# Optimization experiments

Hardware: AMD Instinct MI355X
Metric: run time of the kernel (lower is better)

## Reference

```python
import jax, jax.numpy as jnp
import numpy as np

EMBED_DIM = 1024
NUM_HEADS = 16
HEAD_DIM = EMBED_DIM // NUM_HEADS


def setup_inputs() -> dict:
    key = jax.random.key(0)
    ks = jax.random.split(key, 5)
    s = 1.0 / np.sqrt(EMBED_DIM)
    x = jax.random.normal(ks[0], (2, 2048, EMBED_DIM), dtype=jnp.float32)
    Wq = jax.random.normal(ks[1], (EMBED_DIM, EMBED_DIM), dtype=jnp.float32) * s
    Wk = jax.random.normal(ks[2], (EMBED_DIM, EMBED_DIM), dtype=jnp.float32) * s
    Wv = jax.random.normal(ks[3], (EMBED_DIM, EMBED_DIM), dtype=jnp.float32) * s
    Wo = jax.random.normal(ks[4], (EMBED_DIM, EMBED_DIM), dtype=jnp.float32) * s
    z = jnp.zeros((EMBED_DIM,), dtype=jnp.float32)
    return {"x": x, "Wq": Wq, "bq": z, "Wk": Wk, "bk": z, "Wv": Wv, "bv": z, "Wo": Wo, "bo": z}


def reference(x, Wq, bq, Wk, bk, Wv, bv, Wo, bo):
    B, S, E = x.shape
    H, D = NUM_HEADS, HEAD_DIM
    # projections; weights stored as [in, out] so y = x @ W + b
    q = (x @ Wq + bq).reshape(B, S, H, D).transpose(0, 2, 1, 3)  # [B,H,S,D]
    k = (x @ Wk + bk).reshape(B, S, H, D).transpose(0, 2, 1, 3)
    v = (x @ Wv + bv).reshape(B, S, H, D).transpose(0, 2, 1, 3)
    scores = jnp.einsum('bhqd,bhkd->bhqk', q, k) / jnp.sqrt(jnp.float32(D))
    attn = jax.nn.softmax(scores, axis=-1)
    out = jnp.einsum('bhqk,bhkd->bhqd', attn, v)  # [B,H,S,D]
    out = out.transpose(0, 2, 1, 3).reshape(B, S, E)
    return out @ Wo + bo
```

## Files before the change

### kernel.cpp

```cpp
#include <hip/hip_runtime.h>
#include <cstdint>
#include <cstddef>

typedef __attribute__((ext_vector_type(8))) short bf16x8;
typedef __attribute__((ext_vector_type(4))) float f32x4;
typedef __attribute__((ext_vector_type(16))) float f32x16;
typedef __attribute__((ext_vector_type(4))) unsigned int u32x4;
typedef __attribute__((ext_vector_type(2))) unsigned int u32x2;

__device__ __forceinline__ unsigned short f2bf(float f) {
    union { float f; unsigned int u; } c; c.f = f;
    unsigned int r = c.u + 0x7FFFu + ((c.u >> 16) & 1u);
    return (unsigned short)(r >> 16);
}
__device__ __forceinline__ unsigned int pack2bf(float a, float b) {
    return (unsigned int)f2bf(a) | ((unsigned int)f2bf(b) << 16);
}
__device__ __forceinline__ unsigned int cvtpk(float lo, float hi) {
    unsigned int r;
    asm("v_cvt_pk_bf16_f32 %0, %1, %2" : "=v"(r) : "v"(lo), "v"(hi));
    return r;
}
__device__ __forceinline__ void gload16(const void* g, void* l) {
    __builtin_amdgcn_global_load_lds((const __attribute__((address_space(1))) void*)g,
                                     (__attribute__((address_space(3))) void*)l, 16, 0, 0);
}
__device__ __forceinline__ float tmax16(const f32x16& v) {
    float a0 = fmaxf(v[0], v[1]),   a1 = fmaxf(v[2], v[3]);
    float a2 = fmaxf(v[4], v[5]),   a3 = fmaxf(v[6], v[7]);
    float a4 = fmaxf(v[8], v[9]),   a5 = fmaxf(v[10], v[11]);
    float a6 = fmaxf(v[12], v[13]), a7 = fmaxf(v[14], v[15]);
    float b0 = fmaxf(a0, a1), b1 = fmaxf(a2, a3);
    float b2 = fmaxf(a4, a5), b3 = fmaxf(a6, a7);
    return fmaxf(fmaxf(b0, b1), fmaxf(b2, b3));
}
__device__ __forceinline__ float tsum16(const float* p) {
    float a0 = p[0] + p[1],   a1 = p[2] + p[3];
    float a2 = p[4] + p[5],   a3 = p[6] + p[7];
    float a4 = p[8] + p[9],   a5 = p[10] + p[11];
    float a6 = p[12] + p[13], a7 = p[14] + p[15];
    float b0 = a0 + a1, b1 = a2 + a3, b2 = a4 + a5, b3 = a6 + a7;
    return (b0 + b1) + (b2 + b3);
}

__global__ __launch_bounds__(256) void cvt_kernel(const float* __restrict__ x,
    const float* __restrict__ w0, const float* __restrict__ w1,
    const float* __restrict__ w2, const float* __restrict__ w3,
    unsigned short* __restrict__ xdst, unsigned short* __restrict__ wdst) {
    __shared__ unsigned short sm[64][68];
    const int bid = blockIdx.x;
    const int tid = threadIdx.x;
    if (bid >= 1024) {
        int e = ((bid - 1024) * 256 + tid) * 8;
        const float4* s4 = reinterpret_cast<const float4*>(x + e);
        float4 a = s4[0], b = s4[1];
        u32x4 o;
        o.x = pack2bf(a.x, a.y); o.y = pack2bf(a.z, a.w);
        o.z = pack2bf(b.x, b.y); o.w = pack2bf(b.z, b.w);
        *reinterpret_cast<u32x4*>(xdst + e) = o;
        return;
    }
    int z = bid >> 8, xb = bid & 255;
    const float* src = (z == 0) ? w0 : (z == 1) ? w1 : (z == 2) ? w2 : w3;
    unsigned short* dst = wdst + (size_t)z * 1048576;
    int n0 = (xb & 15) * 64;
    int k0 = (xb >> 4) * 64;
    #pragma unroll
    for (int i = 0; i < 4; i++) {
        int e = i * 1024 + tid * 4;
        int r = e >> 6, c = e & 63;
        float4 v = *reinterpret_cast<const float4*>(src + (size_t)(k0 + r) * 1024 + n0 + c);
        u32x2 p; p.x = pack2bf(v.x, v.y); p.y = pack2bf(v.z, v.w);
        *reinterpret_cast<u32x2*>(&sm[r][c]) = p;
    }
    __syncthreads();
    #pragma unroll
    for (int i = 0; i < 4; i++) {
        int e = i * 1024 + tid * 4;
        int n = e >> 6, kk = e & 63;
        u32x2 p;
        p.x = (unsigned)sm[kk][n]     | ((unsigned)sm[kk + 1][n] << 16);
        p.y = (unsigned)sm[kk + 2][n] | ((unsigned)sm[kk + 3][n] << 16);
        *reinterpret_cast<u32x2*>(dst + (size_t)(n0 + n) * 1024 + k0 + kk) = p;
    }
}

__device__ __forceinline__ void gemm128_main(
    const unsigned short* __restrict__ A, const unsigned short* __restrict__ Wt,
    int m0, int n0, int tid,
    unsigned short* Asm, unsigned short* Bsm,
    f32x4 acc[4][4])
{
    const int lane = tid & 63;
    const int w = tid >> 6;
    const int wm = w >> 1, wn = w & 1;
    const int lr = lane & 15, lg = lane >> 4;
    for (int k0 = 0; k0 < 1024; k0 += 64) {
        __syncthreads();
        #pragma unroll
        for (int i = 0; i < 4; i++) {
            int L = (i * 4 + w) * 64 + lane;
            int r = L >> 3, cs = L & 7;
            int c = cs ^ (r & 7);
            gload16(A  + (size_t)(m0 + r) * 1024 + k0 + c * 8, Asm + (i * 4 + w) * 512);
            gload16(Wt + (size_t)(n0 + r) * 1024 + k0 + c * 8, Bsm + (i * 4 + w) * 512);
        }
        __syncthreads();
        #pragma unroll
        for (int ks = 0; ks < 2; ks++) {
            bf16x8 af[4], bfr[4];
            #pragma unroll
            for (int t = 0; t < 4; t++) {
                int Ra = wm * 64 + t * 16 + lr;
                af[t]  = *reinterpret_cast<const bf16x8*>(Asm + Ra * 64 + ((ks * 4 + lg) ^ (Ra & 7)) * 8);
                int Rb = wn * 64 + t * 16 + lr;
                bfr[t] = *reinterpret_cast<const bf16x8*>(Bsm + Rb * 64 + ((ks * 4 + lg) ^ (Rb & 7)) * 8);
            }
            #pragma unroll
            for (int mt = 0; mt < 4; mt++) {
                #pragma unroll
                for (int nt = 0; nt < 4; nt++)
                    acc[mt][nt] = __builtin_amdgcn_mfma_f32_16x16x32_bf16(af[mt], bfr[nt], acc[mt][nt], 0, 0, 0);
            }
        }
    }
}

__global__ __launch_bounds__(256) void gemm_qkv_kernel(
    const unsigned short* __restrict__ A, const unsigned short* __restrict__ WtBase,
    const float* __restrict__ bq, const float* __restrict__ bk, const float* __restrict__ bv,
    unsigned short* __restrict__ Qo, unsigned short* __restrict__ Ko, unsigned short* __restrict__ Vto)
{
    __shared__ unsigned short Asm[8192];
    __shared__ unsigned short Bsm[8192];
    const int bid = blockIdx.x;
    const int wg = (bid & 7) * 96 + (bid >> 3);
    const int z = wg >> 8;
    const int rem = wg & 255;
    const int m0 = (rem >> 3) * 128, n0 = (rem & 7) * 128;
    const unsigned short* Wt = WtBase + (size_t)z * 1048576;
    const float* bias = (z == 0) ? bq : (z == 1) ? bk : bv;
    const int tid = threadIdx.x, lane = tid & 63, w = tid >> 6;
    const int wm = w >> 1, wn = w & 1, lr = lane & 15, lg = lane >> 4;
    f32x4 acc[4][4];
    f32x4 zero4 = {0.f, 0.f, 0.f, 0.f};
    #pragma unroll
    for (int i = 0; i < 4; i++)
        #pragma unroll
        for (int j = 0; j < 4; j++) acc[i][j] = zero4;
    gemm128_main(A, Wt, m0, n0, tid, Asm, Bsm, acc);

    const float qs = 0.125f * 1.44269504088896341f;
    #pragma unroll
    for (int mt = 0; mt < 4; mt++) {
        #pragma unroll
        for (int nt = 0; nt < 4; nt++) {
            int gn = n0 + wn * 64 + nt * 16 + lr;
            int h = gn >> 6, d = gn & 63;
            int rb = m0 + wm * 64 + mt * 16 + lg * 4;
            int b_ = rb >> 11, s = rb & 2047;
            float bv_ = bias[gn];
            if (z == 2) {
                u32x2 p;
                p.x = pack2bf(acc[mt][nt][0] + bv_, acc[mt][nt][1] + bv_);
                p.y = pack2bf(acc[mt][nt][2] + bv_, acc[mt][nt][3] + bv_);
                *reinterpret_cast<u32x2*>(Vto + ((size_t)(b_ * 16 + h) * 64 + d) * 2048 + s) = p;
            } else {
                unsigned short* dst = (z == 0) ? Qo : Ko;
                float sc_ = (z == 0) ? qs : 1.0f;
                #pragma unroll
                for (int r = 0; r < 4; r++)
                    dst[((size_t)(b_ * 16 + h) * 2048 + (s + r)) * 64 + d] = f2bf((acc[mt][nt][r] + bv_) * sc_);
            }
        }
    }
}

__global__ __launch_bounds__(256, 2) void attn_kernel(
    const unsigned short* __restrict__ Qg,
    const unsigned short* __restrict__ Kg,
    const unsigned short* __restrict__ Vtg,
    unsigned short* __restrict__ Og)
{
    __shared__ unsigned short Ksm[128][72];
    __shared__ unsigned short Vsm[64][136];

    const int tid = threadIdx.x, lane = tid & 63, w = tid >> 6;
    const int l31 = lane & 31, L = lane >> 5;
    const int bh = blockIdx.y, q0 = blockIdx.x * 128;
    const size_t kvbase = (size_t)bh * (2048 * 64);
    const size_t vtbase = (size_t)bh * (64 * 2048);

    {
        u32x4 qr[4];
        #pragma unroll
        for (int i = 0; i < 4; i++) {
            int ck = i * 256 + tid; int r = ck >> 3, c = (ck & 7) * 8;
            qr[i] = *reinterpret_cast<const u32x4*>(Qg + kvbase + (size_t)(q0 + r) * 64 + c);
        }
        #pragma unroll
        for (int i = 0; i < 4; i++) {
            int ck = i * 256 + tid; int r = ck >> 3, c = (ck & 7) * 8;
            *reinterpret_cast<u32x4*>(&Ksm[r][c]) = qr[i];
        }
    }
    __syncthreads();
    bf16x8 qf[4];
    #pragma unroll
    for (int ds = 0; ds < 4; ds++)
        qf[ds] = *reinterpret_cast<const bf16x8*>(&Ksm[w * 32 + l31][ds * 16 + L * 8]);
    __syncthreads();

    f32x16 oacc[2];
    #pragma unroll
    for (int dt = 0; dt < 2; dt++)
        #pragma unroll
        for (int j = 0; j < 16; j++) oacc[dt][j] = 0.f;
    float m_run = -3.0e38f, l_run = 0.f;

    f32x16 z16;
    #pragma unroll
    for (int j = 0; j < 16; j++) z16[j] = 0.f;

    u32x4 kreg[4], vreg[4];
#define LOAD_TILE(KV0)                                                                      \
    _Pragma("unroll")                                                                       \
    for (int i = 0; i < 4; i++) {                                                           \
        int ck = i * 256 + tid; int r = ck >> 3, c = (ck & 7) * 8;                          \
        kreg[i] = *reinterpret_cast<const u32x4*>(Kg + kvbase + (size_t)((KV0) + r) * 64 + c); \
        int dv = ck >> 4, cv = (ck & 15) * 8;                                               \
        vreg[i] = *reinterpret_cast<const u32x4*>(Vtg + vtbase + (size_t)dv * 2048 + (KV0) + cv); \
    }

    LOAD_TILE(0)
    for (int kt = 0; kt < 16; kt++) {
        #pragma unroll
        for (int i = 0; i < 4; i++) {
            int ck = i * 256 + tid; int r = ck >> 3, c = (ck & 7) * 8;
            int rp = r ^ (((((r >> 2) ^ (r >> 3)) & 1)) * 12);
            *reinterpret_cast<u32x4*>(&Ksm[rp][c]) = kreg[i];
            int dv = ck >> 4, cv = (ck & 15) * 8;
            *reinterpret_cast<u32x4*>(&Vsm[dv][cv]) = vreg[i];
        }
        __syncthreads();
        int kvn = (kt < 15) ? (kt + 1) * 128 : 0;
        LOAD_TILE(kvn)

        f32x16 sc[4];
        #pragma unroll
        for (int nt = 0; nt < 4; nt++) {
            {
                bf16x8 kf = *reinterpret_cast<const bf16x8*>(&Ksm[nt * 32 + l31][L * 8]);
                sc[nt] = __builtin_amdgcn_mfma_f32_32x32x16_bf16(kf, qf[0], z16, 0, 0, 0);
            }
            #pragma unroll
            for (int ds = 1; ds < 4; ds++) {
                bf16x8 kf = *reinterpret_cast<const bf16x8*>(&Ksm[nt * 32 + l31][ds * 16 + L * 8]);
                sc[nt] = __builtin_amdgcn_mfma_f32_32x32x16_bf16(kf, qf[ds], sc[nt], 0, 0, 0);
            }
        }

        float pmax = fmaxf(fmaxf(tmax16(sc[0]), tmax16(sc[1])),
                           fmaxf(tmax16(sc[2]), tmax16(sc[3])));
        pmax = fmaxf(pmax, __shfl_xor(pmax, 32));

        if (__any(pmax - m_run > 8.0f)) {
            float mnew = fmaxf(m_run, pmax);
            float f = __builtin_amdgcn_exp2f(m_run - mnew);
            l_run *= f;
            #pragma unroll
            for (int dt = 0; dt < 2; dt++)
                #pragma unroll
                for (int j = 0; j < 16; j++) oacc[dt][j] *= f;
            m_run = mnew;
        }

        float psum = 0.f;
        unsigned pdw[4][4][2];
        #pragma unroll
        for (int nt = 0; nt < 4; nt++) {
            float p[16];
            #pragma unroll
            for (int j = 0; j < 16; j++)
                p[j] = __builtin_amdgcn_exp2f(sc[nt][j] - m_run);
            psum += tsum16(p);
            #pragma unroll
            for (int a = 0; a < 4; a++) {
                pdw[nt][a][0] = cvtpk(p[4 * a + 0], p[4 * a + 1]);
                pdw[nt][a][1] = cvtpk(p[4 * a + 2], p[4 * a + 3]);
            }
        }
        psum += __shfl_xor(psum, 32);
        l_run += psum;

        #pragma unroll
        for (int kt2 = 0; kt2 < 8; kt2++) {
            const int nt = kt2 >> 1, c2 = (kt2 & 1) * 2;
            u32x4 pf4;
            pf4.x = pdw[nt][c2][0];
            pf4.y = pdw[nt][c2][1];
            pf4.z = pdw[nt][c2 + 1][0];
            pf4.w = pdw[nt][c2 + 1][1];
            bf16x8 pfr = *reinterpret_cast<bf16x8*>(&pf4);
            #pragma unroll
            for (int dt = 0; dt < 2; dt++) {
                bf16x8 vf = *reinterpret_cast<const bf16x8*>(&Vsm[dt * 32 + l31][kt2 * 16 + L * 8]);
                oacc[dt] = __builtin_amdgcn_mfma_f32_32x32x16_bf16(vf, pfr, oacc[dt], 0, 0, 0);
            }
        }
        __syncthreads();
    }
#undef LOAD_TILE

    float inv = 1.0f / l_run;
    const int b_ = bh >> 4, h = bh & 15;
    const int s = q0 + w * 32 + l31;
    unsigned short* orow = Og + ((size_t)b_ * 2048 + s) * 1024 + h * 64;
    #pragma unroll
    for (int dt = 0; dt < 2; dt++) {
        #pragma unroll
        for (int g = 0; g < 4; g++) {
            u32x2 pp;
            pp.x = cvtpk(oacc[dt][4 * g + 0] * inv, oacc[dt][4 * g + 1] * inv);
            pp.y = cvtpk(oacc[dt][4 * g + 2] * inv, oacc[dt][4 * g + 3] * inv);
            *reinterpret_cast<u32x2*>(orow + dt * 32 + g * 8 + 4 * L) = pp;
        }
    }
}

__global__ __launch_bounds__(256) void gemm_out_kernel(
    const unsigned short* __restrict__ A, const unsigned short* __restrict__ Wt,
    const float* __restrict__ bias, float* __restrict__ out)
{
    __shared__ unsigned short Asm[8192];
    __shared__ unsigned short Bsm[8192];
    const int bid = blockIdx.x;
    const int wg = (bid & 7) * 32 + (bid >> 3);
    const int m0 = (wg >> 3) * 128, n0 = (wg & 7) * 128;
    const int tid = threadIdx.x, lane = tid & 63, w = tid >> 6;
    const int wm = w >> 1, wn = w & 1, lr = lane & 15, lg = lane >> 4;
    f32x4 acc[4][4];
    f32x4 zero4 = {0.f, 0.f, 0.f, 0.f};
    #pragma unroll
    for (int i = 0; i < 4; i++)
        #pragma unroll
        for (int j = 0; j < 4; j++) acc[i][j] = zero4;
    gemm128_main(A, Wt, m0, n0, tid, Asm, Bsm, acc);
    #pragma unroll
    for (int mt = 0; mt < 4; mt++) {
        #pragma unroll
        for (int nt = 0; nt < 4; nt++) {
            int gn = n0 + wn * 64 + nt * 16 + lr;
            float bv_ = bias[gn];
            int rb = m0 + wm * 64 + mt * 16 + lg * 4;
            #pragma unroll
            for (int r = 0; r < 4; r++)
                out[(size_t)(rb + r) * 1024 + gn] = acc[mt][nt][r] + bv_;
        }
    }
}

extern "C" void kernel_launch(void* const* d_in, const int* in_sizes, int n_in,
                              void* d_out, int out_size, void* d_ws, size_t ws_size,
                              hipStream_t stream) {
    const float* x  = (const float*)d_in[0];
    const float* Wq = (const float*)d_in[1];
    const float* bq = (const float*)d_in[2];
    const float* Wk = (const float*)d_in[3];
    const float* bk = (const float*)d_in[4];
    const float* Wv = (const float*)d_in[5];
    const float* bv = (const float*)d_in[6];
    const float* Wo = (const float*)d_in[7];
    const float* bo = (const float*)d_in[8];
    float* out = (float*)d_out;

    if (ws_size < (size_t)25165824 * 2) return;
    unsigned short* ws  = (unsigned short*)d_ws;
    unsigned short* xbf = ws;
    unsigned short* wt  = ws + 4194304;
    unsigned short* Qb  = ws + 8388608;
    unsigned short* Kb  = ws + 12582912;
    unsigned short* Vtb = ws + 16777216;
    unsigned short* Ob  = ws + 20971520;

    cvt_kernel<<<3072, 256, 0, stream>>>(x, Wq, Wk, Wv, Wo, xbf, wt);
    gemm_qkv_kernel<<<768, 256, 0, stream>>>(xbf, wt, bq, bk, bv, Qb, Kb, Vtb);
    attn_kernel<<<dim3(16, 32), 256, 0, stream>>>(Qb, Kb, Vtb, Ob);
    gemm_out_kernel<<<256, 256, 0, stream>>>(Ob, wt + 3 * 1048576, bo, out);
}
```

Before: 129.1 us.

## Double-buffer GEMM K-loop with 32-wide stages and raise occupancy hint

Restructures the shared GEMM main loop into a two-buffer ping-pong pipeline over K-slices of 32. The next slice is loaded asynchronously into LDS while the current one runs through MFMA, which should hide global-load latency behind compute. The LDS swizzle is changed to match the narrower 32-column rows. Launch bounds now request three blocks per SM for the QKV and output GEMMs, which may force register limits or spills. Barriers per K step rise, and each MFMA round has less work between syncs.

```diff
diff --git a/kernel.cpp b/kernel.cpp
--- a/kernel.cpp
+++ b/kernel.cpp
@@ -85,6 +85,40 @@
     }
 }
 
+__device__ __forceinline__ void gemm128_stage(
+    const unsigned short* __restrict__ A, const unsigned short* __restrict__ Wt,
+    int m0, int n0, int tid, int k0,
+    unsigned short* Ad, unsigned short* Bd)
+{
+    #pragma unroll
+    for (int i = 0; i < 2; i++) {
+        int L = i * 256 + tid;
+        int r = L >> 2, cs = L & 3;
+        int c = cs ^ ((r & 3) ^ ((r >> 2) & 3));
+        gload16(A  + (size_t)(m0 + r) * 1024 + k0 + c * 8, Ad + L * 8);
+        gload16(Wt + (size_t)(n0 + r) * 1024 + k0 + c * 8, Bd + L * 8);
+    }
+}
+__device__ __forceinline__ void gemm128_compute(
+    const unsigned short* Ac, const unsigned short* Bc,
+    int wm, int wn, int lr, int lg,
+    f32x4 acc[4][4])
+{
+    bf16x8 af[4], bfr[4];
+    #pragma unroll
+    for (int t = 0; t < 4; t++) {
+        int Ra = wm * 64 + t * 16 + lr;
+        af[t]  = *reinterpret_cast<const bf16x8*>(Ac + Ra * 32 + (lg ^ ((Ra & 3) ^ ((Ra >> 2) & 3))) * 8);
+        int Rb = wn * 64 + t * 16 + lr;
+        bfr[t] = *reinterpret_cast<const bf16x8*>(Bc + Rb * 32 + (lg ^ ((Rb & 3) ^ ((Rb >> 2) & 3))) * 8);
+    }
+    #pragma unroll
+    for (int mt = 0; mt < 4; mt++) {
+        #pragma unroll
+        for (int nt = 0; nt < 4; nt++)
+            acc[mt][nt] = __builtin_amdgcn_mfma_f32_16x16x32_bf16(af[mt], bfr[nt], acc[mt][nt], 0, 0, 0);
+    }
+}
 __device__ __forceinline__ void gemm128_main(
     const unsigned short* __restrict__ A, const unsigned short* __restrict__ Wt,
     int m0, int n0, int tid,
@@ -95,38 +129,23 @@
     const int w = tid >> 6;
     const int wm = w >> 1, wn = w & 1;
     const int lr = lane & 15, lg = lane >> 4;
-    for (int k0 = 0; k0 < 1024; k0 += 64) {
+    unsigned short* A0 = Asm;        unsigned short* B0 = Bsm;
+    unsigned short* A1 = Asm + 4096; unsigned short* B1 = Bsm + 4096;
+
+    gemm128_stage(A, Wt, m0, n0, tid, 0, A0, B0);
+    __syncthreads();
+    for (int t = 0; t < 32; t += 2) {
+        gemm128_stage(A, Wt, m0, n0, tid, (t + 1) * 32, A1, B1);
+        gemm128_compute(A0, B0, wm, wn, lr, lg, acc);
         __syncthreads();
-        #pragma unroll
-        for (int i = 0; i < 4; i++) {
-            int L = (i * 4 + w) * 64 + lane;
-            int r = L >> 3, cs = L & 7;
-            int c = cs ^ (r & 7);
-            gload16(A  + (size_t)(m0 + r) * 1024 + k0 + c * 8, Asm + (i * 4 + w) * 512);
-            gload16(Wt + (size_t)(n0 + r) * 1024 + k0 + c * 8, Bsm + (i * 4 + w) * 512);
-        }
+        if (t + 2 < 32)
+            gemm128_stage(A, Wt, m0, n0, tid, (t + 2) * 32, A0, B0);
+        gemm128_compute(A1, B1, wm, wn, lr, lg, acc);
         __syncthreads();
-        #pragma unroll
-        for (int ks = 0; ks < 2; ks++) {
-            bf16x8 af[4], bfr[4];
-            #pragma unroll
-            for (int t = 0; t < 4; t++) {
-                int Ra = wm * 64 + t * 16 + lr;
-                af[t]  = *reinterpret_cast<const bf16x8*>(Asm + Ra * 64 + ((ks * 4 + lg) ^ (Ra & 7)) * 8);
-                int Rb = wn * 64 + t * 16 + lr;
-                bfr[t] = *reinterpret_cast<const bf16x8*>(Bsm + Rb * 64 + ((ks * 4 + lg) ^ (Rb & 7)) * 8);
-            }
-            #pragma unroll
-            for (int mt = 0; mt < 4; mt++) {
-                #pragma unroll
-                for (int nt = 0; nt < 4; nt++)
-                    acc[mt][nt] = __builtin_amdgcn_mfma_f32_16x16x32_bf16(af[mt], bfr[nt], acc[mt][nt], 0, 0, 0);
-            }
-        }
-    }
-}
-
-__global__ __launch_bounds__(256) void gemm_qkv_kernel(
+    }
+}
+
+__global__ __launch_bounds__(256, 3) void gemm_qkv_kernel(
     const unsigned short* __restrict__ A, const unsigned short* __restrict__ WtBase,
     const float* __restrict__ bq, const float* __restrict__ bk, const float* __restrict__ bv,
     unsigned short* __restrict__ Qo, unsigned short* __restrict__ Ko, unsigned short* __restrict__ Vto)
@@ -328,7 +347,7 @@
     }
 }
 
-__global__ __launch_bounds__(256) void gemm_out_kernel(
+__global__ __launch_bounds__(256, 3) void gemm_out_kernel(
     const unsigned short* __restrict__ A, const unsigned short* __restrict__ Wt,
     const float* __restrict__ bias, float* __restrict__ out)
 {
```

Measured after the change: 122.6 us. 1.05x faster.
